# Kernel tuning notes

Hardware: AMD Instinct MI355X
Metric: run time of the kernel (lower is better)

## Reference

```python
import jax, jax.numpy as jnp
import numpy as np

WS = 8   # window_size
SS = 4   # shift_size
NH = 6   # num_heads
EPS = 1e-5


def _win_partition(x, ws):
    # x: [B, H, W, C] -> [B * H/ws * W/ws, ws*ws, C]
    B, H, W, C = x.shape
    x = x.reshape(B, H // ws, ws, W // ws, ws, C)
    return x.transpose(0, 1, 3, 2, 4, 5).reshape(-1, ws * ws, C)


def _win_reverse(wins, ws, H, W, B):
    C = wins.shape[-1]
    x = wins.reshape(B, H // ws, W // ws, ws, ws, C)
    return x.transpose(0, 1, 3, 2, 4, 5).reshape(B, H, W, C)


def _rel_pos_index(ws):
    # static numpy computation, identical to the torch buffer
    coords = np.stack(np.meshgrid(np.arange(ws), np.arange(ws), indexing='ij')).reshape(2, -1)
    rel = coords[:, :, None] - coords[:, None, :]          # [2, N, N]
    rel = rel.transpose(1, 2, 0).copy()                    # [N, N, 2]
    rel[..., 0] += ws - 1
    rel[..., 1] += ws - 1
    rel[..., 0] *= 2 * ws - 1
    return rel.sum(-1)                                     # [N, N] int


def _attn_mask_np(H, W, ws, ss):
    # static numpy computation of the SW-MSA mask, identical to _compute_mask
    img = np.zeros((1, H, W, 1), np.float32)
    cnt = 0
    for hs in (slice(0, -ws), slice(-ws, -ss), slice(-ss, None)):
        for wsl in (slice(0, -ws), slice(-ws, -ss), slice(-ss, None)):
            img[:, hs, wsl, :] = cnt
            cnt += 1
    mw = img.reshape(1, H // ws, ws, W // ws, ws, 1).transpose(0, 1, 3, 2, 4, 5).reshape(-1, ws * ws)
    am = mw[:, None, :] - mw[:, :, None]                   # [nW, N, N]
    return np.where(am != 0, np.float32(-100.0), np.float32(0.0))


def _swin_forward(x, qkv_w, qkv_b, proj_w, proj_b, rpb_table,
                  norm2_g, norm2_b, mlp_w1, mlp_b1, mlp_w2, mlp_b2, H, W):
    B, L, C = x.shape
    ws, ss, nh = WS, SS, NH
    hd = C // nh
    x2d = x.reshape(B, H, W, C)
    shifted = jnp.roll(x2d, (-ss, -ss), axis=(1, 2))
    win = _win_partition(shifted, ws)                      # [B_, N, C]
    B_, N, _ = win.shape

    # --- window attention (note: original applies attention to un-normalized x) ---
    qkv = (win @ qkv_w + qkv_b).reshape(B_, N, 3, nh, hd)
    q = qkv[:, :, 0].transpose(0, 2, 1, 3)                 # [B_, nh, N, hd]
    k = qkv[:, :, 1].transpose(0, 2, 1, 3)
    v = qkv[:, :, 2].transpose(0, 2, 1, 3)
    attn = jnp.einsum('bhnd,bhmd->bhnm', q, k) * (hd ** -0.5)

    bias = rpb_table[jnp.asarray(_rel_pos_index(ws)).reshape(-1)]
    bias = bias.reshape(N, N, nh).transpose(2, 0, 1)       # [nh, N, N]
    attn = attn + bias[None]

    mask = jnp.asarray(_attn_mask_np(H, W, ws, ss))        # [nW, N, N]
    nW = mask.shape[0]
    attn = attn.reshape(B_ // nW, nW, nh, N, N) + mask[None, :, None]
    attn = jax.nn.softmax(attn.reshape(B_, nh, N, N), axis=-1)

    out = jnp.einsum('bhnm,bhmd->bnhd', attn, v).reshape(B_, N, C)
    out = out @ proj_w + proj_b

    x2d = _win_reverse(out, ws, H, W, B)
    x2d = jnp.roll(x2d, (ss, ss), axis=(1, 2))
    x = x + x2d.reshape(B, L, C)

    # --- MLP branch with LayerNorm (norm2) ---
    mu = x.mean(-1, keepdims=True)
    var = x.var(-1, keepdims=True)
    xn = (x - mu) * jax.lax.rsqrt(var + EPS) * norm2_g + norm2_b
    h = jax.nn.gelu(xn @ mlp_w1 + mlp_b1, approximate=False)
    return x + (h @ mlp_w2 + mlp_b2)


def setup_inputs() -> dict:
    B, H, W, C = 8, 128, 128, 192
    mlp_hidden = 4 * C
    ks = jax.random.split(jax.random.key(0), 6)
    std = 0.02
    return {
        'x': jax.random.normal(ks[0], (B, H * W, C), jnp.float32),
        'qkv_w': jax.random.normal(ks[1], (C, 3 * C), jnp.float32) * std,
        'qkv_b': jnp.zeros((3 * C,), jnp.float32),
        'proj_w': jax.random.normal(ks[2], (C, C), jnp.float32) * std,
        'proj_b': jnp.zeros((C,), jnp.float32),
        'rpb_table': jax.random.normal(ks[3], ((2 * WS - 1) ** 2, NH), jnp.float32) * std,
        'norm2_g': jnp.ones((C,), jnp.float32),
        'norm2_b': jnp.zeros((C,), jnp.float32),
        'mlp_w1': jax.random.normal(ks[4], (C, mlp_hidden), jnp.float32) * std,
        'mlp_b1': jnp.zeros((mlp_hidden,), jnp.float32),
        'mlp_w2': jax.random.normal(ks[5], (mlp_hidden, C), jnp.float32) * std,
        'mlp_b2': jnp.zeros((C,), jnp.float32),
        'H': H,
        'W': W,
    }


def reference(x, qkv_w, qkv_b, proj_w, proj_b, rpb_table, norm2_g, norm2_b,
              mlp_w1, mlp_b1, mlp_w2, mlp_b2, H, W):
    return _swin_forward(x, qkv_w, qkv_b, proj_w, proj_b, rpb_table,
                         norm2_g, norm2_b, mlp_w1, mlp_b1, mlp_w2, mlp_b2, H, W)
```

## Files before the change

### kernel.cpp

```cpp
#include <hip/hip_runtime.h>
#include <hip/hip_bf16.h>


typedef __hip_bfloat16 bf16;
typedef __attribute__((ext_vector_type(8))) short bfrag;
typedef __attribute__((ext_vector_type(4))) float ffrag;

union bfu { bf16 h[8]; bfrag v; };

__device__ __forceinline__ float b2f(bf16 v) { return __bfloat162float(v); }
__device__ __forceinline__ bf16  f2b(float v) { return __float2bfloat16(v); }

#define MFMA(a, b, c) __builtin_amdgcn_mfma_f32_16x16x32_bf16((a), (b), (c), 0, 0, 0)

#define WS_XRES  0ULL
#define WS_OG    100663296ULL
#define WS_QKVTG 150994944ULL
#define WS_QBG   151250944ULL
#define WS_PROJT 151253504ULL
#define WS_W1T   151330304ULL
#define WS_W2T   151637504ULL
#define WS_SB    151969280ULL

__device__ __forceinline__ void stage_lds(const void* g, void* l, int nbytes, int t) {
    const int lane16 = (t & 63) * 16;
    for (int base = (t >> 6) * 1024; base < nbytes; base += 4096) {
        if (base + lane16 < nbytes) {
            __builtin_amdgcn_global_load_lds(
                (const __attribute__((address_space(1))) void*)((const char*)g + base + lane16),
                (__attribute__((address_space(3))) void*)((char*)l + base),
                16, 0, 0);
        }
    }
}

__device__ __forceinline__ float gelu_t(float x) {
    float y = x * (1.5957691216057308f + 0.07135481627f * x * x);
    return x * (1.f / (1.f + __expf(-y)));
}

__global__ __launch_bounds__(256) void k_prep(
    const float* __restrict__ qkv_w, const float* __restrict__ qkv_b,
    const float* __restrict__ proj_w, const float* __restrict__ w1,
    const float* __restrict__ w2, const float* __restrict__ rpb,
    char* __restrict__ ws)
{
    int i = blockIdx.x * 256 + threadIdx.x;
    bf16*  qkvTg = (bf16*)(ws + WS_QKVTG);
    float* qbg   = (float*)(ws + WS_QBG);
    bf16*  projT = (bf16*)(ws + WS_PROJT);
    bf16*  w1T   = (bf16*)(ws + WS_W1T);
    bf16*  w2T   = (bf16*)(ws + WS_W2T);
    bf16*  sbB   = (bf16*)(ws + WS_SB);

    if (i < 128000) {
        int g = i / 64000, rem = i % 64000;
        int c = rem / 200, k = rem % 200;
        float v = 0.f;
        if (k < 192) {
            if (c < 96)       v = qkv_w[k * 576 + g * 96 + c];
            else if (c < 192) v = qkv_w[k * 576 + 192 + g * 96 + (c - 96)];
            else if (c < 288) v = qkv_w[k * 576 + 384 + g * 96 + (c - 192)];
        }
        qkvTg[i] = f2b(v);
    } else if (i < 128640) {
        int j = i - 128000;
        int g = j / 320, c = j % 320;
        float v = 0.f;
        if (c < 96)       v = qkv_b[g * 96 + c];
        else if (c < 192) v = qkv_b[192 + g * 96 + (c - 96)];
        else if (c < 288) v = qkv_b[384 + g * 96 + (c - 192)];
        qbg[j] = v;
    } else if (i < 167040) {
        int j = i - 128640;
        int c = j / 200, k = j % 200;
        projT[j] = f2b(k < 192 ? proj_w[k * 192 + c] : 0.f);
    } else if (i < 320640) {
        int j = i - 167040;
        int c = j / 200, k = j % 200;
        w1T[j] = f2b(k < 192 ? w1[k * 768 + c] : 0.f);
    } else if (i < 486528) {
        int j = i - 320640;
        int kc = j / 13824, r = (j % 13824) / 72, kk = j % 72;
        w2T[j] = f2b(kk < 64 ? w2[(kc * 64 + kk) * 192 + r] : 0.f);
    } else if (i < 584832) {
        int j = i - 486528;
        int cls = j / 24576, h = (j % 24576) / 4096;
        int ii = (j % 4096) / 64, jj = j % 64;
        int ri = ii >> 3, ci = ii & 7, rj = jj >> 3, cj = jj & 7;
        float bias = rpb[(((ri - rj + 7) * 15) + (ci - cj + 7)) * 6 + h];
        int clsR = cls >> 1, clsC = cls & 1;
        int regi = (clsR ? (ri < 4 ? 1 : 2) : 0) * 3 + (clsC ? (ci < 4 ? 1 : 2) : 0);
        int regj = (clsR ? (rj < 4 ? 1 : 2) : 0) * 3 + (clsC ? (cj < 4 ? 1 : 2) : 0);
        sbB[j] = f2b(bias + (regi == regj ? 0.f : -100.f));
    }
}

__global__ __launch_bounds__(256, 2) void k_attn(
    const float* __restrict__ x, const char* __restrict__ ws,
    bf16* __restrict__ Og)
{
    __shared__ __align__(16) unsigned char smem[75264];
    bf16* sW  = (bf16*)(smem);
    bf16* sQ  = (bf16*)(smem + 25600);
    bf16* sK  = (bf16*)(smem + 38912);
    bf16* sVT = (bf16*)(smem + 52224);
    bf16* sP  = (bf16*)(smem + 66048);

    const bf16*  qkvTg = (const bf16*)(ws + WS_QKVTG);
    const float* qbg   = (const float*)(ws + WS_QBG);
    const bf16*  sbB   = (const bf16*)(ws + WS_SB);

    const int t    = threadIdx.x;
    const int lane = t & 63, quad = lane >> 4, l15 = lane & 15;
    const int wave = t >> 6, r0 = wave * 16;
    const int win = blockIdx.x;
    const int b   = win >> 8;
    const int wi  = win & 255;
    const int wh  = wi >> 4, wwi = wi & 15;

    bfrag aX[6];
    {
        int row = r0 + l15;
        int rr = row >> 3, cc = row & 7;
        int hs  = (wh * 8 + rr + 4) & 127;
        int wsx = (wwi * 8 + cc + 4) & 127;
        const float* xrow = x + ((size_t)(b * 16384 + hs * 128 + wsx)) * 192;
        #pragma unroll
        for (int kb = 0; kb < 6; kb++) {
            float4 f0 = *(const float4*)(xrow + kb * 32 + quad * 8);
            float4 f1 = *(const float4*)(xrow + kb * 32 + quad * 8 + 4);
            bfu u;
            u.h[0] = f2b(f0.x); u.h[1] = f2b(f0.y); u.h[2] = f2b(f0.z); u.h[3] = f2b(f0.w);
            u.h[4] = f2b(f1.x); u.h[5] = f2b(f1.y); u.h[6] = f2b(f1.z); u.h[7] = f2b(f1.w);
            aX[kb] = u.v;
        }
    }

    const int cls = ((wh == 15) ? 2 : 0) + ((wwi == 15) ? 1 : 0);
    const bf16* bBc = sbB + (size_t)cls * 24576;
    bf16* sPw = sP + wave * 16 * 72;

    for (int g = 0; g < 2; g++) {
        for (int ch = 0; ch < 5; ch++) {
            __syncthreads();
            stage_lds(qkvTg + (size_t)(g * 320 + ch * 64) * 200, sW, 25600, t);
            __syncthreads();
            #pragma unroll
            for (int ct = 0; ct < 4; ct++) {
                int c0 = ch * 64 + ct * 16;
                if (c0 < 288) {
                    bfrag bw[6];
                    #pragma unroll
                    for (int kb = 0; kb < 6; kb++)
                        bw[kb] = *(const bfrag*)&sW[(ct * 16 + l15) * 200 + kb * 32 + quad * 8];
                    ffrag acc = {0.f, 0.f, 0.f, 0.f};
                    #pragma unroll
                    for (int kb = 0; kb < 6; kb++) acc = MFMA(aX[kb], bw[kb], acc);
                    float bias = qbg[g * 320 + c0 + l15];
                    #pragma unroll
                    for (int reg = 0; reg < 4; reg++) {
                        int r = r0 + quad * 4 + reg;
                        float v = acc[reg] + bias;
                        if (c0 < 96)       sQ[r * 104 + c0 + l15] = f2b(v);
                        else if (c0 < 192) sK[r * 104 + (c0 - 96) + l15] = f2b(v);
                        else               sVT[(c0 - 192 + l15) * 72 + r] = f2b(v);
                    }
                }
            }
        }
        __syncthreads();
        for (int hl = 0; hl < 3; hl++) {
            int h = g * 3 + hl;
            bfrag aQ = *(const bfrag*)&sQ[(r0 + l15) * 104 + hl * 32 + quad * 8];
            ffrag Sf[4];
            #pragma unroll
            for (int jt = 0; jt < 4; jt++) {
                bfrag bK = *(const bfrag*)&sK[(jt * 16 + l15) * 104 + hl * 32 + quad * 8];
                ffrag z = {0.f, 0.f, 0.f, 0.f};
                Sf[jt] = MFMA(aQ, bK, z);
            }
            const bf16* bb = bBc + h * 4096 + (r0 + quad * 4) * 64 + l15;
            #pragma unroll
            for (int jt = 0; jt < 4; jt++)
                #pragma unroll
                for (int reg = 0; reg < 4; reg++)
                    Sf[jt][reg] = Sf[jt][reg] * 0.1767766952966369f
                                + b2f(bb[reg * 64 + jt * 16]);
            #pragma unroll
            for (int reg = 0; reg < 4; reg++) {
                float m = fmaxf(fmaxf(Sf[0][reg], Sf[1][reg]), fmaxf(Sf[2][reg], Sf[3][reg]));
                m = fmaxf(m, __shfl_xor(m, 1)); m = fmaxf(m, __shfl_xor(m, 2));
                m = fmaxf(m, __shfl_xor(m, 4)); m = fmaxf(m, __shfl_xor(m, 8));
                float s = 0.f;
                #pragma unroll
                for (int jt = 0; jt < 4; jt++) { Sf[jt][reg] = __expf(Sf[jt][reg] - m); s += Sf[jt][reg]; }
                s += __shfl_xor(s, 1); s += __shfl_xor(s, 2);
                s += __shfl_xor(s, 4); s += __shfl_xor(s, 8);
                float inv = 1.f / s;
                int prow = (quad * 4 + reg) * 72;
                #pragma unroll
                for (int jt = 0; jt < 4; jt++)
                    sPw[prow + jt * 16 + l15] = f2b(Sf[jt][reg] * inv);
            }
            bfrag aP0 = *(const bfrag*)&sPw[l15 * 72 + quad * 8];
            bfrag aP1 = *(const bfrag*)&sPw[l15 * 72 + 32 + quad * 8];
            #pragma unroll
            for (int ct = 0; ct < 2; ct++) {
                bfrag bV0 = *(const bfrag*)&sVT[(hl * 32 + ct * 16 + l15) * 72 + quad * 8];
                bfrag bV1 = *(const bfrag*)&sVT[(hl * 32 + ct * 16 + l15) * 72 + 32 + quad * 8];
                ffrag z = {0.f, 0.f, 0.f, 0.f};
                ffrag o = MFMA(aP1, bV1, MFMA(aP0, bV0, z));
                #pragma unroll
                for (int reg = 0; reg < 4; reg++)
                    Og[((size_t)win * 64 + r0 + quad * 4 + reg) * 192 + h * 32 + ct * 16 + l15]
                        = f2b(o[reg]);
            }
        }
    }
}

__global__ __launch_bounds__(256, 2) void k_proj(
    const float* __restrict__ x, const float* __restrict__ proj_b,
    const char* __restrict__ ws, float* __restrict__ xres)
{
    __shared__ __align__(16) bf16 sWp[192 * 200];

    const bf16* projT = (const bf16*)(ws + WS_PROJT);
    const bf16* Og    = (const bf16*)(ws + WS_OG);

    const int t    = threadIdx.x;
    const int lane = t & 63, quad = lane >> 4, l15 = lane & 15;
    const int wave = t >> 6, r0 = wave * 32;
    const size_t row0 = (size_t)blockIdx.x * 128;

    stage_lds(projT, sWp, 76800, t);

    bfrag aO[2][6];
    #pragma unroll
    for (int rt = 0; rt < 2; rt++)
        #pragma unroll
        for (int kb = 0; kb < 6; kb++)
            aO[rt][kb] = *(const bfrag*)&Og[(row0 + r0 + rt * 16 + l15) * 192 + kb * 32 + quad * 8];

    size_t tokb[2][4];
    #pragma unroll
    for (int rt = 0; rt < 2; rt++)
        #pragma unroll
        for (int reg = 0; reg < 4; reg++) {
            int n = r0 + rt * 16 + quad * 4 + reg;
            int w2 = (int)(blockIdx.x * 2) + (n >> 6);
            int nl = n & 63;
            int b = w2 >> 8, wi = w2 & 255;
            int wh = wi >> 4, wwi = wi & 15;
            int sr = wh * 8 + (nl >> 3), sc = wwi * 8 + (nl & 7);
            int h2 = (sr + 4) & 127, w2c = (sc + 4) & 127;
            tokb[rt][reg] = ((size_t)(b * 16384 + h2 * 128 + w2c)) * 192;
        }

    __syncthreads();

    ffrag acc[2][12];
    #pragma unroll
    for (int rt = 0; rt < 2; rt++)
        #pragma unroll
        for (int ct = 0; ct < 12; ct++)
            acc[rt][ct] = (ffrag){0.f, 0.f, 0.f, 0.f};

    #pragma unroll
    for (int ct = 0; ct < 12; ct++) {
        bfrag bw[6];
        #pragma unroll
        for (int kb = 0; kb < 6; kb++)
            bw[kb] = *(const bfrag*)&sWp[(ct * 16 + l15) * 200 + kb * 32 + quad * 8];
        #pragma unroll
        for (int rt = 0; rt < 2; rt++)
            #pragma unroll
            for (int kb = 0; kb < 6; kb++)
                acc[rt][ct] = MFMA(aO[rt][kb], bw[kb], acc[rt][ct]);
    }

    #pragma unroll
    for (int rt = 0; rt < 2; rt++)
        #pragma unroll
        for (int ct = 0; ct < 12; ct++) {
            int col = ct * 16 + l15;
            float pb = proj_b[col];
            #pragma unroll
            for (int reg = 0; reg < 4; reg++) {
                size_t gi = tokb[rt][reg] + col;
                xres[gi] = acc[rt][ct][reg] + pb + x[gi];
            }
        }
}

__global__ __launch_bounds__(256, 2) void k_mlp(
    const float* __restrict__ xres, const float* __restrict__ g,
    const float* __restrict__ bb, const float* __restrict__ b1,
    const float* __restrict__ b2, const char* __restrict__ ws,
    float* __restrict__ out)
{
    __shared__ __align__(16) unsigned char smem[71680];
    bf16* U   = (bf16*)(smem);
    bf16* W2s = (bf16*)(smem + 25600);
    bf16* hS  = (bf16*)(smem + 53248);

    const bf16* w1T = (const bf16*)(ws + WS_W1T);
    const bf16* w2T = (const bf16*)(ws + WS_W2T);

    const int t    = threadIdx.x;
    const int lane = t & 63, quad = lane >> 4, l15 = lane & 15;
    const int wave = t >> 6, r0 = wave * 32;
    const size_t row0 = (size_t)blockIdx.x * 128;

    #pragma unroll
    for (int p = 0; p < 2; p++) {
        int row = r0 + p * 16 + l15;
        const float4* src = (const float4*)(xres + (row0 + row) * 192 + quad * 48);
        float v[48];
        float s = 0.f, sq = 0.f;
        #pragma unroll
        for (int u = 0; u < 12; u++) {
            float4 f = src[u];
            v[u*4] = f.x; v[u*4+1] = f.y; v[u*4+2] = f.z; v[u*4+3] = f.w;
            s  += f.x + f.y + f.z + f.w;
            sq += f.x*f.x + f.y*f.y + f.z*f.z + f.w*f.w;
        }
        s  += __shfl_xor(s, 16);  s  += __shfl_xor(s, 32);
        sq += __shfl_xor(sq, 16); sq += __shfl_xor(sq, 32);
        float mean = s * (1.f / 192.f);
        float var  = sq * (1.f / 192.f) - mean * mean;
        float rstd = rsqrtf(var + 1e-5f);
        __hip_bfloat162* dst = (__hip_bfloat162*)&U[row * 200 + quad * 48];
        #pragma unroll
        for (int u = 0; u < 24; u++) {
            int c = quad * 48 + u * 2;
            float a0 = (v[u*2]   - mean) * rstd * g[c]     + bb[c];
            float a1 = (v[u*2+1] - mean) * rstd * g[c + 1] + bb[c + 1];
            dst[u] = __float22bfloat162_rn({a0, a1});
        }
    }

    bfrag aX[2][6];
    #pragma unroll
    for (int rt = 0; rt < 2; rt++)
        #pragma unroll
        for (int kb = 0; kb < 6; kb++)
            aX[rt][kb] = *(const bfrag*)&U[(r0 + rt*16 + l15) * 200 + kb*32 + quad*8];

    __syncthreads();

    bf16* hs_w = hS + wave * 32 * 72;

    ffrag oacc[2][12];
    #pragma unroll
    for (int rt = 0; rt < 2; rt++)
        #pragma unroll
        for (int ct = 0; ct < 12; ct++)
            oacc[rt][ct] = (ffrag){0.f, 0.f, 0.f, 0.f};

    for (int kc = 0; kc < 12; kc++) {
        __syncthreads();
        stage_lds(w1T + (size_t)kc * 64 * 200, U, 25600, t);
        stage_lds(w2T + (size_t)kc * 13824, W2s, 27648, t);
        __syncthreads();

        #pragma unroll
        for (int ct = 0; ct < 4; ct++) {
            bfrag bw[6];
            #pragma unroll
            for (int kb = 0; kb < 6; kb++)
                bw[kb] = *(const bfrag*)&U[(ct*16 + l15) * 200 + kb*32 + quad*8];
            float bias = b1[kc * 64 + ct * 16 + l15];
            #pragma unroll
            for (int rt = 0; rt < 2; rt++) {
                ffrag a = {0.f, 0.f, 0.f, 0.f};
                #pragma unroll
                for (int kb = 0; kb < 6; kb++) a = MFMA(aX[rt][kb], bw[kb], a);
                #pragma unroll
                for (int reg = 0; reg < 4; reg++)
                    hs_w[(rt*16 + quad*4 + reg) * 72 + ct*16 + l15] =
                        f2b(gelu_t(a[reg] + bias));
            }
        }
        bfrag aH[2][2];
        #pragma unroll
        for (int rt = 0; rt < 2; rt++)
            #pragma unroll
            for (int k0 = 0; k0 < 2; k0++)
                aH[rt][k0] = *(const bfrag*)&hs_w[(rt*16 + l15) * 72 + k0*32 + quad*8];
        #pragma unroll
        for (int ct = 0; ct < 12; ct++) {
            bfrag bw2[2];
            #pragma unroll
            for (int k0 = 0; k0 < 2; k0++)
                bw2[k0] = *(const bfrag*)&W2s[(ct*16 + l15) * 72 + k0*32 + quad*8];
            #pragma unroll
            for (int rt = 0; rt < 2; rt++)
                #pragma unroll
                for (int k0 = 0; k0 < 2; k0++)
                    oacc[rt][ct] = MFMA(aH[rt][k0], bw2[k0], oacc[rt][ct]);
        }
    }

    #pragma unroll
    for (int rt = 0; rt < 2; rt++)
        #pragma unroll
        for (int ct = 0; ct < 12; ct++) {
            int col = ct * 16 + l15;
            float b2v = b2[col];
            #pragma unroll
            for (int reg = 0; reg < 4; reg++) {
                size_t gi = (row0 + r0 + rt*16 + quad*4 + reg) * 192 + col;
                out[gi] = xres[gi] + oacc[rt][ct][reg] + b2v;
            }
        }
}

extern "C" void kernel_launch(void* const* d_in, const int* in_sizes, int n_in,
                              void* d_out, int out_size, void* d_ws, size_t ws_size,
                              hipStream_t stream)
{
    (void)in_sizes; (void)n_in; (void)out_size; (void)ws_size;

    const float* x      = (const float*)d_in[0];
    const float* qkv_w  = (const float*)d_in[1];
    const float* qkv_b  = (const float*)d_in[2];
    const float* proj_w = (const float*)d_in[3];
    const float* proj_b = (const float*)d_in[4];
    const float* rpb    = (const float*)d_in[5];
    const float* n2g    = (const float*)d_in[6];
    const float* n2b    = (const float*)d_in[7];
    const float* w1     = (const float*)d_in[8];
    const float* b1     = (const float*)d_in[9];
    const float* w2     = (const float*)d_in[10];
    const float* b2     = (const float*)d_in[11];

    char*  ws   = (char*)d_ws;
    float* xres = (float*)(ws + WS_XRES);
    bf16*  Og   = (bf16*)(ws + WS_OG);
    float* out  = (float*)d_out;

    hipLaunchKernelGGL(k_prep, dim3(2285), dim3(256), 0, stream,
                       qkv_w, qkv_b, proj_w, w1, w2, rpb, ws);
    hipLaunchKernelGGL(k_attn, dim3(2048), dim3(256), 0, stream,
                       x, ws, Og);
    hipLaunchKernelGGL(k_proj, dim3(1024), dim3(256), 0, stream,
                       x, proj_b, ws, xres);
    hipLaunchKernelGGL(k_mlp,  dim3(1024), dim3(256), 0, stream,
                       xres, n2g, n2b, b1, b2, ws, out);
}
```

Before: 471.2 us.

## Double-buffer weight staging in attention and MLP kernels with smaller chunks

Splits the QKV weight staging in the attention kernel and the W1/W2 staging in the MLP kernel into half-size chunks held in ping-pong LDS buffers. The next chunk is prefetched with async global-to-LDS loads while the current one feeds the MFMAs, which leaves one barrier per chunk instead of two. Biases are also staged into LDS, and the W2 layout is repacked to 32-wide K chunks with a new padding. In exchange there are twice as many loop iterations and barriers, and LDS use and occupancy change slightly.

```diff
diff --git a/kernel.cpp b/kernel.cpp
--- a/kernel.cpp
+++ b/kernel.cpp
@@ -20,7 +20,7 @@
 #define WS_PROJT 151253504ULL
 #define WS_W1T   151330304ULL
 #define WS_W2T   151637504ULL
-#define WS_SB    151969280ULL
+#define WS_SB    152006144ULL
 
 __device__ __forceinline__ void stage_lds(const void* g, void* l, int nbytes, int t) {
     const int lane16 = (t & 63) * 16;
@@ -79,12 +79,12 @@
         int j = i - 167040;
         int c = j / 200, k = j % 200;
         w1T[j] = f2b(k < 192 ? w1[k * 768 + c] : 0.f);
-    } else if (i < 486528) {
+    } else if (i < 504960) {
         int j = i - 320640;
-        int kc = j / 13824, r = (j % 13824) / 72, kk = j % 72;
-        w2T[j] = f2b(kk < 64 ? w2[(kc * 64 + kk) * 192 + r] : 0.f);
-    } else if (i < 584832) {
-        int j = i - 486528;
+        int kc = j / 7680, r = (j % 7680) / 40, kk = j % 40;
+        w2T[j] = f2b(kk < 32 ? w2[(kc * 32 + kk) * 192 + r] : 0.f);
+    } else if (i < 603264) {
+        int j = i - 504960;
         int cls = j / 24576, h = (j % 24576) / 4096;
         int ii = (j % 4096) / 64, jj = j % 64;
         int ri = ii >> 3, ci = ii & 7, rj = jj >> 3, cj = jj & 7;
@@ -100,12 +100,13 @@
     const float* __restrict__ x, const char* __restrict__ ws,
     bf16* __restrict__ Og)
 {
-    __shared__ __align__(16) unsigned char smem[75264];
-    bf16* sW  = (bf16*)(smem);
-    bf16* sQ  = (bf16*)(smem + 25600);
-    bf16* sK  = (bf16*)(smem + 38912);
-    bf16* sVT = (bf16*)(smem + 52224);
-    bf16* sP  = (bf16*)(smem + 66048);
+    __shared__ __align__(16) unsigned char smem[77824];
+    bf16*  sWb = (bf16*)(smem);
+    bf16*  sQ  = (bf16*)(smem + 25600);
+    bf16*  sK  = (bf16*)(smem + 38912);
+    bf16*  sVT = (bf16*)(smem + 52224);
+    bf16*  sP  = (bf16*)(smem + 66048);
+    float* sQB = (float*)(smem + 75264);
 
     const bf16*  qkvTg = (const bf16*)(ws + WS_QKVTG);
     const float* qbg   = (const float*)(ws + WS_QBG);
@@ -119,6 +120,9 @@
     const int wi  = win & 255;
     const int wh  = wi >> 4, wwi = wi & 15;
 
+    stage_lds(qbg, smem + 75264, 2560, t);
+    stage_lds(qkvTg, sWb, 12800, t);
+
     bfrag aX[6];
     {
         int row = r0 + l15;
@@ -141,35 +145,41 @@
     const bf16* bBc = sbB + (size_t)cls * 24576;
     bf16* sPw = sP + wave * 16 * 72;
 
+    __syncthreads();
+
+    int pb = 0;
     for (int g = 0; g < 2; g++) {
-        for (int ch = 0; ch < 5; ch++) {
+        for (int c = 0; c < 9; c++) {
+            if (c < 8)
+                stage_lds(qkvTg + (size_t)(g * 320 + (c + 1) * 32) * 200,
+                          sWb + (pb ^ 1) * 6400, 12800, t);
+            else if (g == 0)
+                stage_lds(qkvTg + (size_t)320 * 200,
+                          sWb + (pb ^ 1) * 6400, 12800, t);
+            const bf16* sW = sWb + pb * 6400;
+            #pragma unroll
+            for (int ct = 0; ct < 2; ct++) {
+                int c0 = c * 32 + ct * 16;
+                bfrag bw[6];
+                #pragma unroll
+                for (int kb = 0; kb < 6; kb++)
+                    bw[kb] = *(const bfrag*)&sW[(ct * 16 + l15) * 200 + kb * 32 + quad * 8];
+                ffrag acc = {0.f, 0.f, 0.f, 0.f};
+                #pragma unroll
+                for (int kb = 0; kb < 6; kb++) acc = MFMA(aX[kb], bw[kb], acc);
+                float bias = sQB[g * 320 + c0 + l15];
+                #pragma unroll
+                for (int reg = 0; reg < 4; reg++) {
+                    int r = r0 + quad * 4 + reg;
+                    float v = acc[reg] + bias;
+                    if (c0 < 96)       sQ[r * 104 + c0 + l15] = f2b(v);
+                    else if (c0 < 192) sK[r * 104 + (c0 - 96) + l15] = f2b(v);
+                    else               sVT[(c0 - 192 + l15) * 72 + r] = f2b(v);
+                }
+            }
             __syncthreads();
-            stage_lds(qkvTg + (size_t)(g * 320 + ch * 64) * 200, sW, 25600, t);
-            __syncthreads();
-            #pragma unroll
-            for (int ct = 0; ct < 4; ct++) {
-                int c0 = ch * 64 + ct * 16;
-                if (c0 < 288) {
-                    bfrag bw[6];
-                    #pragma unroll
-                    for (int kb = 0; kb < 6; kb++)
-                        bw[kb] = *(const bfrag*)&sW[(ct * 16 + l15) * 200 + kb * 32 + quad * 8];
-                    ffrag acc = {0.f, 0.f, 0.f, 0.f};
-                    #pragma unroll
-                    for (int kb = 0; kb < 6; kb++) acc = MFMA(aX[kb], bw[kb], acc);
-                    float bias = qbg[g * 320 + c0 + l15];
-                    #pragma unroll
-                    for (int reg = 0; reg < 4; reg++) {
-                        int r = r0 + quad * 4 + reg;
-                        float v = acc[reg] + bias;
-                        if (c0 < 96)       sQ[r * 104 + c0 + l15] = f2b(v);
-                        else if (c0 < 192) sK[r * 104 + (c0 - 96) + l15] = f2b(v);
-                        else               sVT[(c0 - 192 + l15) * 72 + r] = f2b(v);
-                    }
-                }
-            }
-        }
-        __syncthreads();
+            pb ^= 1;
+        }
         for (int hl = 0; hl < 3; hl++) {
             int h = g * 3 + hl;
             bfrag aQ = *(const bfrag*)&sQ[(r0 + l15) * 104 + hl * 32 + quad * 8];
@@ -217,6 +227,7 @@
                         = f2b(o[reg]);
             }
         }
+        __syncthreads();
     }
 }
 
@@ -300,10 +311,12 @@
     const float* __restrict__ b2, const char* __restrict__ ws,
     float* __restrict__ out)
 {
-    __shared__ __align__(16) unsigned char smem[71680];
-    bf16* U   = (bf16*)(smem);
-    bf16* W2s = (bf16*)(smem + 25600);
-    bf16* hS  = (bf16*)(smem + 53248);
+    __shared__ __align__(16) unsigned char smem[69632];
+    bf16*  w1base = (bf16*)(smem);
+    bf16*  w2base = (bf16*)(smem + 25600);
+    bf16*  hS     = (bf16*)(smem + 56320);
+    float* sB1f   = (float*)(smem + 66560);
+    bf16*  U      = (bf16*)(smem);
 
     const bf16* w1T = (const bf16*)(ws + WS_W1T);
     const bf16* w2T = (const bf16*)(ws + WS_W2T);
@@ -312,6 +325,8 @@
     const int lane = t & 63, quad = lane >> 4, l15 = lane & 15;
     const int wave = t >> 6, r0 = wave * 32;
     const size_t row0 = (size_t)blockIdx.x * 128;
+
+    stage_lds(b1, smem + 66560, 3072, t);
 
     #pragma unroll
     for (int p = 0; p < 2; p++) {
@@ -350,7 +365,11 @@
 
     __syncthreads();
 
-    bf16* hs_w = hS + wave * 32 * 72;
+    stage_lds(w1T, w1base, 12800, t);
+    stage_lds(w2T, w2base, 15360, t);
+    __syncthreads();
+
+    bf16* hs_w = hS + wave * 32 * 40;
 
     ffrag oacc[2][12];
     #pragma unroll
@@ -359,19 +378,22 @@
         for (int ct = 0; ct < 12; ct++)
             oacc[rt][ct] = (ffrag){0.f, 0.f, 0.f, 0.f};
 
-    for (int kc = 0; kc < 12; kc++) {
-        __syncthreads();
-        stage_lds(w1T + (size_t)kc * 64 * 200, U, 25600, t);
-        stage_lds(w2T + (size_t)kc * 13824, W2s, 27648, t);
-        __syncthreads();
-
-        #pragma unroll
-        for (int ct = 0; ct < 4; ct++) {
+    for (int kc = 0; kc < 24; kc++) {
+        const int p = kc & 1;
+        const bf16* w1c = w1base + p * 6400;
+        const bf16* w2c = w2base + p * 7680;
+        if (kc < 23) {
+            stage_lds(w1T + (size_t)(kc + 1) * 6400, w1base + (p ^ 1) * 6400, 12800, t);
+            stage_lds(w2T + (size_t)(kc + 1) * 7680, w2base + (p ^ 1) * 7680, 15360, t);
+        }
+
+        #pragma unroll
+        for (int ct = 0; ct < 2; ct++) {
             bfrag bw[6];
             #pragma unroll
             for (int kb = 0; kb < 6; kb++)
-                bw[kb] = *(const bfrag*)&U[(ct*16 + l15) * 200 + kb*32 + quad*8];
-            float bias = b1[kc * 64 + ct * 16 + l15];
+                bw[kb] = *(const bfrag*)&w1c[(ct*16 + l15) * 200 + kb*32 + quad*8];
+            float bias = sB1f[kc * 32 + ct * 16 + l15];
             #pragma unroll
             for (int rt = 0; rt < 2; rt++) {
                 ffrag a = {0.f, 0.f, 0.f, 0.f};
@@ -379,28 +401,22 @@
                 for (int kb = 0; kb < 6; kb++) a = MFMA(aX[rt][kb], bw[kb], a);
                 #pragma unroll
                 for (int reg = 0; reg < 4; reg++)
-                    hs_w[(rt*16 + quad*4 + reg) * 72 + ct*16 + l15] =
+                    hs_w[(rt*16 + quad*4 + reg) * 40 + ct*16 + l15] =
                         f2b(gelu_t(a[reg] + bias));
             }
         }
-        bfrag aH[2][2];
+        bfrag aH[2];
         #pragma unroll
         for (int rt = 0; rt < 2; rt++)
-            #pragma unroll
-            for (int k0 = 0; k0 < 2; k0++)
-                aH[rt][k0] = *(const bfrag*)&hs_w[(rt*16 + l15) * 72 + k0*32 + quad*8];
+            aH[rt] = *(const bfrag*)&hs_w[(rt*16 + l15) * 40 + quad*8];
         #pragma unroll
         for (int ct = 0; ct < 12; ct++) {
-            bfrag bw2[2];
-            #pragma unroll
-            for (int k0 = 0; k0 < 2; k0++)
-                bw2[k0] = *(const bfrag*)&W2s[(ct*16 + l15) * 72 + k0*32 + quad*8];
+            bfrag bw2 = *(const bfrag*)&w2c[(ct*16 + l15) * 40 + quad*8];
             #pragma unroll
             for (int rt = 0; rt < 2; rt++)
-                #pragma unroll
-                for (int k0 = 0; k0 < 2; k0++)
-                    oacc[rt][ct] = MFMA(aH[rt][k0], bw2[k0], oacc[rt][ct]);
-        }
+                oacc[rt][ct] = MFMA(aH[rt], bw2, oacc[rt][ct]);
+        }
+        __syncthreads();
     }
 
     #pragma unroll
@@ -441,7 +457,7 @@
     bf16*  Og   = (bf16*)(ws + WS_OG);
     float* out  = (float*)d_out;
 
-    hipLaunchKernelGGL(k_prep, dim3(2285), dim3(256), 0, stream,
+    hipLaunchKernelGGL(k_prep, dim3(2357), dim3(256), 0, stream,
                        qkv_w, qkv_b, proj_w, w1, w2, rpb, ws);
     hipLaunchKernelGGL(k_attn, dim3(2048), dim3(256), 0, stream,
                        x, ws, Og);
```

Measured after the change: 482.8 us. +2.5%, slower.

## Double-buffer per-head QKV weight chunks in attention kernel to cut LDS and raise occupancy

Applied to the files above, without the earlier changes.

Reorders the prepared QKV weight layout so that each head's Q, K and V columns are contiguous in 32-column chunks. The attention kernel then processes one head at a time, streaming 32-column weight chunks through a double-buffered LDS region, with the next chunk's copy issued before computing on the current one. LDS per block shrinks from about 75KB to 52KB and launch bounds go from 2 to 3 blocks per CU, meant to raise occupancy and overlap the weight staging with the MFMA work. In exchange there are more __syncthreads per window (18 chunks instead of 10) and a smaller GEMM granularity per stage.

```diff
diff --git a/kernel.cpp b/kernel.cpp
--- a/kernel.cpp
+++ b/kernel.cpp
@@ -57,19 +57,25 @@
         int g = i / 64000, rem = i % 64000;
         int c = rem / 200, k = rem % 200;
         float v = 0.f;
-        if (k < 192) {
-            if (c < 96)       v = qkv_w[k * 576 + g * 96 + c];
-            else if (c < 192) v = qkv_w[k * 576 + 192 + g * 96 + (c - 96)];
-            else if (c < 288) v = qkv_w[k * 576 + 384 + g * 96 + (c - 192)];
+        if (k < 192 && c < 288) {
+            int h = g * 3 + c / 96, j = c % 96;
+            int src = (j < 32) ? (h * 32 + j)
+                    : (j < 64) ? (192 + h * 32 + (j - 32))
+                               : (384 + h * 32 + (j - 64));
+            v = qkv_w[k * 576 + src];
         }
         qkvTg[i] = f2b(v);
     } else if (i < 128640) {
         int j = i - 128000;
         int g = j / 320, c = j % 320;
         float v = 0.f;
-        if (c < 96)       v = qkv_b[g * 96 + c];
-        else if (c < 192) v = qkv_b[192 + g * 96 + (c - 96)];
-        else if (c < 288) v = qkv_b[384 + g * 96 + (c - 192)];
+        if (c < 288) {
+            int h = g * 3 + c / 96, jj = c % 96;
+            int src = (jj < 32) ? (h * 32 + jj)
+                    : (jj < 64) ? (192 + h * 32 + (jj - 32))
+                                : (384 + h * 32 + (jj - 64));
+            v = qkv_b[src];
+        }
         qbg[j] = v;
     } else if (i < 167040) {
         int j = i - 128640;
@@ -96,16 +102,17 @@
     }
 }
 
-__global__ __launch_bounds__(256, 2) void k_attn(
+__global__ __launch_bounds__(256, 3) void k_attn(
     const float* __restrict__ x, const char* __restrict__ ws,
     bf16* __restrict__ Og)
 {
-    __shared__ __align__(16) unsigned char smem[75264];
-    bf16* sW  = (bf16*)(smem);
-    bf16* sQ  = (bf16*)(smem + 25600);
-    bf16* sK  = (bf16*)(smem + 38912);
-    bf16* sVT = (bf16*)(smem + 52224);
-    bf16* sP  = (bf16*)(smem + 66048);
+    __shared__ __align__(16) unsigned char smem[52224];
+    bf16*  sWb = (bf16*)(smem);
+    bf16*  sQh = (bf16*)(smem + 25600);
+    bf16*  sKh = (bf16*)(smem + 30720);
+    bf16*  sVT = (bf16*)(smem + 35840);
+    bf16*  sP  = (bf16*)(smem + 40448);
+    float* sQB = (float*)(smem + 49664);
 
     const bf16*  qkvTg = (const bf16*)(ws + WS_QKVTG);
     const float* qbg   = (const float*)(ws + WS_QBG);
@@ -119,6 +126,9 @@
     const int wi  = win & 255;
     const int wh  = wi >> 4, wwi = wi & 15;
 
+    stage_lds(qbg, smem + 49664, 2560, t);
+    stage_lds(qkvTg, sWb, 12800, t);
+
     bfrag aX[6];
     {
         int row = r0 + l15;
@@ -141,42 +151,47 @@
     const bf16* bBc = sbB + (size_t)cls * 24576;
     bf16* sPw = sP + wave * 16 * 72;
 
-    for (int g = 0; g < 2; g++) {
-        for (int ch = 0; ch < 5; ch++) {
-            __syncthreads();
-            stage_lds(qkvTg + (size_t)(g * 320 + ch * 64) * 200, sW, 25600, t);
-            __syncthreads();
-            #pragma unroll
-            for (int ct = 0; ct < 4; ct++) {
-                int c0 = ch * 64 + ct * 16;
-                if (c0 < 288) {
-                    bfrag bw[6];
-                    #pragma unroll
-                    for (int kb = 0; kb < 6; kb++)
-                        bw[kb] = *(const bfrag*)&sW[(ct * 16 + l15) * 200 + kb * 32 + quad * 8];
-                    ffrag acc = {0.f, 0.f, 0.f, 0.f};
-                    #pragma unroll
-                    for (int kb = 0; kb < 6; kb++) acc = MFMA(aX[kb], bw[kb], acc);
-                    float bias = qbg[g * 320 + c0 + l15];
-                    #pragma unroll
-                    for (int reg = 0; reg < 4; reg++) {
-                        int r = r0 + quad * 4 + reg;
-                        float v = acc[reg] + bias;
-                        if (c0 < 96)       sQ[r * 104 + c0 + l15] = f2b(v);
-                        else if (c0 < 192) sK[r * 104 + (c0 - 96) + l15] = f2b(v);
-                        else               sVT[(c0 - 192 + l15) * 72 + r] = f2b(v);
-                    }
-                }
+    __syncthreads();
+
+    int pb = 0;
+    int cb = 0;
+    for (int cc = 0; cc < 18; cc++) {
+        const int h = cc / 3, cpart = cc - h * 3;
+        if (cc < 17) {
+            int cbn = (cc == 8) ? 320 : cb + 32;
+            stage_lds(qkvTg + (size_t)cbn * 200, sWb + (pb ^ 1) * 6400, 12800, t);
+        }
+        const bf16* sW = sWb + pb * 6400;
+        #pragma unroll
+        for (int ct = 0; ct < 2; ct++) {
+            bfrag bw[6];
+            #pragma unroll
+            for (int kb = 0; kb < 6; kb++)
+                bw[kb] = *(const bfrag*)&sW[(ct * 16 + l15) * 200 + kb * 32 + quad * 8];
+            ffrag acc = {0.f, 0.f, 0.f, 0.f};
+            #pragma unroll
+            for (int kb = 0; kb < 6; kb++) acc = MFMA(aX[kb], bw[kb], acc);
+            float bias = sQB[cb + ct * 16 + l15];
+            const int cl = ct * 16 + l15;
+            #pragma unroll
+            for (int reg = 0; reg < 4; reg++) {
+                int r = r0 + quad * 4 + reg;
+                float v = acc[reg] + bias;
+                if (cpart == 0)      sQh[r * 40 + cl] = f2b(v);
+                else if (cpart == 1) sKh[r * 40 + cl] = f2b(v);
+                else                 sVT[cl * 72 + r] = f2b(v);
             }
         }
         __syncthreads();
-        for (int hl = 0; hl < 3; hl++) {
-            int h = g * 3 + hl;
-            bfrag aQ = *(const bfrag*)&sQ[(r0 + l15) * 104 + hl * 32 + quad * 8];
+        pb ^= 1;
+        cb = (cc == 8) ? 320 : cb + 32;
+
+        if (cpart == 2) {
+            bfrag aQ = *(const bfrag*)&sQh[(r0 + l15) * 40 + quad * 8];
             ffrag Sf[4];
             #pragma unroll
             for (int jt = 0; jt < 4; jt++) {
-                bfrag bK = *(const bfrag*)&sK[(jt * 16 + l15) * 104 + hl * 32 + quad * 8];
+                bfrag bK = *(const bfrag*)&sKh[(jt * 16 + l15) * 40 + quad * 8];
                 ffrag z = {0.f, 0.f, 0.f, 0.f};
                 Sf[jt] = MFMA(aQ, bK, z);
             }
@@ -207,8 +222,8 @@
             bfrag aP1 = *(const bfrag*)&sPw[l15 * 72 + 32 + quad * 8];
             #pragma unroll
             for (int ct = 0; ct < 2; ct++) {
-                bfrag bV0 = *(const bfrag*)&sVT[(hl * 32 + ct * 16 + l15) * 72 + quad * 8];
-                bfrag bV1 = *(const bfrag*)&sVT[(hl * 32 + ct * 16 + l15) * 72 + 32 + quad * 8];
+                bfrag bV0 = *(const bfrag*)&sVT[(ct * 16 + l15) * 72 + quad * 8];
+                bfrag bV1 = *(const bfrag*)&sVT[(ct * 16 + l15) * 72 + 32 + quad * 8];
                 ffrag z = {0.f, 0.f, 0.f, 0.f};
                 ffrag o = MFMA(aP1, bV1, MFMA(aP0, bV0, z));
                 #pragma unroll
@@ -216,6 +231,7 @@
                     Og[((size_t)win * 64 + r0 + quad * 4 + reg) * 192 + h * 32 + ct * 16 + l15]
                         = f2b(o[reg]);
             }
+            if (cc < 17) __syncthreads();
         }
     }
 }
```

After: 479.0 us. No clear change (+1.6%).
